# Performance work log

Hardware: AMD Instinct MI355X
Metric: run time of the kernel (lower is better)

## Reference

```python
import jax, jax.numpy as jnp
import numpy as np

EPS = 1e-5  # torch InstanceNorm2d default eps


def conv1x1(x, w, b):
    # x: [B,C,H,W], w: [O,C], b: [O]
    return jnp.einsum('bchw,oc->bohw', x, w) + b[None, :, None, None]


def conv3x3(x, w, b):
    y = jax.lax.conv_general_dilated(x, w, (1, 1), 'SAME',
                                     dimension_numbers=('NCHW', 'OIHW', 'NCHW'))
    return y + b[None, :, None, None]


def inorm(x):
    # InstanceNorm2d, affine=False, biased variance
    m = jnp.mean(x, axis=(2, 3), keepdims=True)
    v = jnp.var(x, axis=(2, 3), keepdims=True)
    return (x - m) * jax.lax.rsqrt(v + EPS)


def self_attn(x, wq, bq, wk, bk, wv, bv, gamma):
    B, C, H, W = x.shape
    N = H * W
    q = conv1x1(x, wq, bq).reshape(B, -1, N)   # [B,C/8,N]
    k = conv1x1(x, wk, bk).reshape(B, -1, N)   # [B,C/8,N]
    A = jax.nn.softmax(jnp.einsum('bdn,bdm->bnm', q, k), axis=-1)  # [B,N,N]
    v = conv1x1(x, wv, bv).reshape(B, C, N)    # [B,C,N]
    out = jnp.einsum('bcm,bnm->bcn', v, A).reshape(B, C, H, W)
    return gamma * out + x


def setup_inputs() -> dict:
    key = jax.random.key(0)
    B, C, H, W = 2, 256, 64, 64
    C8 = C // 8
    ks = iter(jax.random.split(key, 40))

    def n(shape, scale=0.05):
        return jax.random.normal(next(ks), shape, dtype=jnp.float32) * scale

    inp = {
        'x': jax.random.normal(next(ks), (B, C, H, W), dtype=jnp.float32),
        'y': jax.random.normal(next(ks), (B, C, H, W), dtype=jnp.float32),
    }
    for p in ('sa1', 'sa2', 'top'):
        inp[p + '_wq'] = n((C8, C)); inp[p + '_bq'] = n((C8,))
        inp[p + '_wk'] = n((C8, C)); inp[p + '_bk'] = n((C8,))
        inp[p + '_wv'] = n((C, C));  inp[p + '_bv'] = n((C,))
        inp[p + '_gamma'] = n((1,), 0.1)
    inp['conv1_w'] = n((C, C, 3, 3)); inp['conv1_b'] = n((C,))
    inp['conv2_w'] = n((C, C, 3, 3)); inp['conv2_b'] = n((C,))
    return inp


def reference(x, y,
              sa1_wq, sa1_bq, sa1_wk, sa1_bk, sa1_wv, sa1_bv, sa1_gamma,
              sa2_wq, sa2_bq, sa2_wk, sa2_bk, sa2_wv, sa2_bv, sa2_gamma,
              top_wq, top_bq, top_wk, top_bk, top_wv, top_bv, top_gamma,
              conv1_w, conv1_b, conv2_w, conv2_b):
    out_1 = inorm(self_attn(x, sa1_wq, sa1_bq, sa1_wk, sa1_bk, sa1_wv, sa1_bv, sa1_gamma))
    out_2 = inorm(out_1 + conv3x3(out_1, conv1_w, conv1_b))
    out_3 = inorm(self_attn(y, sa2_wq, sa2_bq, sa2_wk, sa2_bk, sa2_wv, sa2_bv, sa2_gamma))

    B, C, H, W = out_2.shape
    N = H * W
    q = conv1x1(out_2, top_wq, top_bq).reshape(B, -1, N)
    k = conv1x1(out_2, top_wk, top_bk).reshape(B, -1, N)
    A = jax.nn.softmax(jnp.einsum('bdn,bdm->bnm', q, k), axis=-1)
    v = conv1x1(out_3, top_wv, top_bv).reshape(B, C, N)
    out = jnp.einsum('bcm,bnm->bcn', v, A).reshape(B, C, H, W)
    out = top_gamma * out + y
    out = inorm(out)
    out = inorm(out + out_3)
    out_4 = conv3x3(out, conv2_w, conv2_b)
    out = inorm(out + out_4)
    return out
```

## Files before the change

### kernel.cpp

```cpp
#include <hip/hip_runtime.h>
#include <hip/hip_bf16.h>

typedef __hip_bfloat16 bf16;
typedef __attribute__((ext_vector_type(8))) short s8v;
typedef __attribute__((ext_vector_type(4))) short s4v;
typedef __attribute__((ext_vector_type(4))) float f4v;

#define NPIX 4096
#define CDIM 256
#define MN_ELEMS (1 << 20)
#define QKVSTR (320L * NPIX)
#define QKTSTR (64L * NPIX)
#define CNL ((long)CDIM * NPIX)

#if __has_builtin(__builtin_amdgcn_exp2f)
#define EXP2F(x) __builtin_amdgcn_exp2f(x)
#else
#define EXP2F(x) exp2f(x)
#endif

typedef __attribute__((address_space(1))) const unsigned int g_u32;
typedef __attribute__((address_space(3))) unsigned int l_u32;
__device__ __forceinline__ void glds16(const void* g, void* l) {
  __builtin_amdgcn_global_load_lds((g_u32*)g, (l_u32*)l, 16, 0, 0);
}

__device__ inline s8v ld8(const bf16* p) { return *(const s8v*)p; }
__device__ inline s8v ld8(const float* p) {
  float4 f0 = *(const float4*)p;
  float4 f1 = *(const float4*)(p + 4);
  s8v r; bf16* e = (bf16*)&r;
  e[0] = __float2bfloat16(f0.x); e[1] = __float2bfloat16(f0.y);
  e[2] = __float2bfloat16(f0.z); e[3] = __float2bfloat16(f0.w);
  e[4] = __float2bfloat16(f1.x); e[5] = __float2bfloat16(f1.y);
  e[6] = __float2bfloat16(f1.z); e[7] = __float2bfloat16(f1.w);
  return r;
}

template<int CB>
__global__ __launch_bounds__(512) void fattn_k(
    const bf16* __restrict__ qkt, const bf16* __restrict__ Vg,
    bf16* __restrict__ out)
{
  constexpr int SC = CB / 64;
  __shared__ bf16 k_s[2][128 * 32];
  __shared__ bf16 v_s[4 * CB * 32];
  __shared__ bf16 p_s[4 * 64 * 32];
  __shared__ float sums[4 * 64];

  const int tid = threadIdx.x;
  const int z = blockIdx.z;
  const int w = tid >> 6, lane = tid & 63;
  const int l15 = lane & 15, oct = lane >> 4;
  const int wr2 = w >> 2, wc2 = w & 3;
  const int pc = w >> 1, pn = w & 1;
  const int n0 = blockIdx.x * 64, c0 = blockIdx.y * CB;
  const bf16* qk = qkt + (long)z * QKTSTR;
  const bf16* Vz = Vg + (long)z * QKVSTR;

  const int t2 = tid >> 2;
  const int kq3 = ((tid & 3) ^ ((t2 >> 1) & 3)) * 8;
  const int vrow = t2 & (CB - 1);
  const int vq3 = ((tid & 3) ^ ((vrow >> 1) & 3)) * 8;

  auto stageK = [&](int m, int buf) {
    glds16(qk + (long)(m + t2) * 64 + 32 + kq3, &k_s[buf][tid * 8]);
  };
  auto stageV = [&](int m) {
    #pragma unroll
    for (int it = 0; it < CB / 32; ++it) {
      const int flat = it * 4096 + tid * 8;
      const int g = flat / (CB * 32);
      glds16(Vz + (long)(c0 + vrow) * 4096 + m + g * 32 + vq3, v_s + flat);
    }
  };

  if (tid < 256)
    glds16(qk + (long)(n0 + t2) * 64 + kq3, p_s + tid * 8);
  stageK(0, 0);
  stageV(0);
  __syncthreads();

  s8v qf[2];
  #pragma unroll
  for (int st = 0; st < 2; ++st) {
    const int row = wr2 * 32 + st * 16 + l15;
    int byte = row * 64 + oct * 16;
    byte ^= ((row >> 1) & 3) << 4;
    qf[st] = *(const s8v*)((const char*)p_s + byte);
  }
  __syncthreads();

  f4v acc[SC][2];
  #pragma unroll
  for (int i = 0; i < SC; ++i)
    #pragma unroll
    for (int j = 0; j < 2; ++j) acc[i][j] = (f4v){0.f, 0.f, 0.f, 0.f};
  float rs[2] = {0.f, 0.f};

  for (int i = 0; i < 32; ++i) {
    const int cur = i & 1;
    if (i < 31) stageK((i + 1) * 128, cur ^ 1);

    s8v kf[2];
    #pragma unroll
    for (int nt = 0; nt < 2; ++nt) {
      const int row = wc2 * 32 + nt * 16 + l15;
      int byte = row * 64 + oct * 16;
      byte ^= ((row >> 1) & 3) << 4;
      kf[nt] = *(const s8v*)((const char*)&k_s[cur][0] + byte);
    }
    #pragma unroll
    for (int st = 0; st < 2; ++st) {
      const int n = wr2 * 32 + st * 16 + l15;
      const int sw = ((n >> 1) & 3) << 4;
      f4v sa[2];
      __builtin_amdgcn_s_setprio(1);
      #pragma unroll
      for (int nt = 0; nt < 2; ++nt) {
        f4v zz = (f4v){0.f, 0.f, 0.f, 0.f};
        sa[nt] = __builtin_amdgcn_mfma_f32_16x16x32_bf16(kf[nt], qf[st], zz, 0, 0, 0);
      }
      __builtin_amdgcn_s_setprio(0);
      #pragma unroll
      for (int nt = 0; nt < 2; ++nt) {
        int byte = wc2 * 4096 + n * 64 + nt * 32 + oct * 8;
        byte ^= sw;
        s4v pk; bf16* pe = (bf16*)&pk;
        float rsum = 0.f;
        #pragma unroll
        for (int r = 0; r < 4; ++r) {
          float e = EXP2F(sa[nt][r]);
          rsum += e;
          pe[r] = __float2bfloat16(e);
        }
        rs[st] += rsum;
        *(s4v*)((char*)p_s + byte) = pk;
      }
    }
    if (i < 31) asm volatile("s_waitcnt vmcnt(1) lgkmcnt(0)" ::: "memory");
    else        asm volatile("s_waitcnt vmcnt(0) lgkmcnt(0)" ::: "memory");
    __builtin_amdgcn_sched_barrier(0);
    __builtin_amdgcn_s_barrier();

    #pragma unroll
    for (int kk = 0; kk < 4; ++kk) {
      s8v vf[SC], pf[2];
      #pragma unroll
      for (int st = 0; st < SC; ++st) {
        const int row = pc * (CB / 4) + st * 16 + l15;
        int byte = kk * (CB * 64) + row * 64 + oct * 16;
        byte ^= ((row >> 1) & 3) << 4;
        vf[st] = *(const s8v*)((const char*)v_s + byte);
      }
      #pragma unroll
      for (int nt = 0; nt < 2; ++nt) {
        const int n = pn * 32 + nt * 16 + l15;
        int byte = kk * 4096 + n * 64 + oct * 16;
        byte ^= ((n >> 1) & 3) << 4;
        pf[nt] = *(const s8v*)((const char*)p_s + byte);
      }
      __builtin_amdgcn_s_setprio(1);
      #pragma unroll
      for (int st = 0; st < SC; ++st)
        #pragma unroll
        for (int nt = 0; nt < 2; ++nt)
          acc[st][nt] = __builtin_amdgcn_mfma_f32_16x16x32_bf16(vf[st], pf[nt], acc[st][nt], 0, 0, 0);
      __builtin_amdgcn_s_setprio(0);
    }
    asm volatile("s_waitcnt vmcnt(0)" ::: "memory");
    __builtin_amdgcn_sched_barrier(0);
    __builtin_amdgcn_s_barrier();

    if (i < 31) stageV((i + 1) * 128);
  }

  #pragma unroll
  for (int st = 0; st < 2; ++st) {
    rs[st] += __shfl_xor(rs[st], 16);
    rs[st] += __shfl_xor(rs[st], 32);
  }
  if (lane < 16) {
    #pragma unroll
    for (int st = 0; st < 2; ++st)
      sums[wc2 * 64 + wr2 * 32 + st * 16 + l15] = rs[st];
  }
  __syncthreads();

  float rinv[2];
  #pragma unroll
  for (int nt = 0; nt < 2; ++nt) {
    const int n = pn * 32 + nt * 16 + l15;
    rinv[nt] = 1.f / (sums[n] + sums[64 + n] + sums[128 + n] + sums[192 + n]);
  }
  bf16* op = out + (long)z * CNL;
  #pragma unroll
  for (int st = 0; st < SC; ++st) {
    const int gc = c0 + pc * (CB / 4) + st * 16 + oct * 4;
    #pragma unroll
    for (int nt = 0; nt < 2; ++nt) {
      const int gn = n0 + pn * 32 + nt * 16 + l15;
      #pragma unroll
      for (int r = 0; r < 4; ++r)
        op[(long)(gc + r) * NPIX + gn] = __float2bfloat16(acc[st][nt][r] * rinv[nt]);
    }
  }
}

__global__ __launch_bounds__(512) void conv_k(
    const bf16* __restrict__ x, const bf16* __restrict__ wcvt,
    const float* __restrict__ bias, bf16* __restrict__ out)
{
  __shared__ bf16 lds[3 * 66 * 66];
  const int tid = threadIdx.x;
  const int h = blockIdx.x;
  const int o0 = blockIdx.y * 128;
  x   += (long)blockIdx.z * CDIM * NPIX;
  out += (long)blockIdx.z * CDIM * NPIX;

  const int w = tid >> 6, lane = tid & 63;
  const int l15 = lane & 15, oct = lane >> 4;

  if (tid < 192) {
    int row = tid >> 6, c = tid & 63;
    lds[(row * 66 + 0) * 66 + c] = __float2bfloat16(0.f);
    lds[(row * 66 + 65) * 66 + c] = __float2bfloat16(0.f);
  }

  f4v acc[4];
  #pragma unroll
  for (int nf = 0; nf < 4; ++nf) acc[nf] = (f4v){0.f, 0.f, 0.f, 0.f};

  const int w2 = tid & 31, chi = tid >> 5;
  const long arow = (long)(o0 + w * 16 + l15) * 2304;

  for (int cg = 0; cg < 4; ++cg) {
    __syncthreads();
    #pragma unroll
    for (int it = 0; it < 12; ++it) {
      int row = it >> 2, cgi = it & 3;
      int c = cgi * 16 + chi;
      int hh = h + row - 1;
      unsigned int pix = 0;
      if ((unsigned)hh < 64u)
        pix = *(const unsigned int*)(x + (long)(cg * 64 + c) * 4096 + hh * 64 + w2 * 2);
      const bf16* pp = (const bf16*)&pix;
      lds[(row * 66 + (w2 * 2 + 1)) * 66 + c] = pp[0];
      lds[(row * 66 + (w2 * 2 + 2)) * 66 + c] = pp[1];
    }
    __syncthreads();

    #pragma unroll
    for (int j = 0; j < 9; ++j) {
      const int dy = j / 3, dx = j % 3;
      #pragma unroll
      for (int kc = 0; kc < 2; ++kc) {
        s8v af = *(const s8v*)(wcvt + arow + j * 256 + cg * 64 + kc * 32 + oct * 8);
        s8v bfv[4];
        #pragma unroll
        for (int nf = 0; nf < 4; ++nf)
          bfv[nf] = *(const s8v*)&lds[(dy * 66 + (nf * 16 + l15 + dx)) * 66 + kc * 32 + oct * 8];
        #pragma unroll
        for (int nf = 0; nf < 4; ++nf)
          acc[nf] = __builtin_amdgcn_mfma_f32_16x16x32_bf16(af, bfv[nf], acc[nf], 0, 0, 0);
      }
    }
  }

  #pragma unroll
  for (int nf = 0; nf < 4; ++nf) {
    const int gn = h * 64 + nf * 16 + l15;
    const int go = o0 + w * 16 + oct * 4;
    #pragma unroll
    for (int r = 0; r < 4; ++r)
      out[(long)(go + r) * NPIX + gn] = __float2bfloat16(acc[nf][r] + bias[go + r]);
  }
}

template<int QKT, typename TBe>
__global__ __launch_bounds__(256) void proj_k(
    const float* __restrict__ A, const float* __restrict__ A2,
    const TBe* __restrict__ B1, const TBe* __restrict__ B2,
    const float* __restrict__ bias, const float* __restrict__ bias2,
    bf16* __restrict__ Cm, bf16* __restrict__ qkt,
    int M, int N, int K, long bbat, long cbat, int nchunk)
{
  __shared__ bf16 a_s[64][40];
  __shared__ bf16 b_s[64][40];
  const int tid = threadIdx.x;
  const int z = blockIdx.z, stage = z >> 1, bat = z & 1;
  const float* Au = stage ? A2 : A;
  const float* biasu = stage ? bias2 : bias;
  const TBe* Bm = (stage ? B2 : B1) + bat * bbat;
  Cm += z * cbat;
  if (QKT) qkt += z * QKTSTR;
  const int m0 = blockIdx.y * 64, n0 = blockIdx.x * 64;
  const int w = tid >> 6, lane = tid & 63;
  const int l15 = lane & 15, oct = lane >> 4;

  f4v acc[4];
  #pragma unroll
  for (int i = 0; i < 4; ++i) acc[i] = (f4v){0.f, 0.f, 0.f, 0.f};

  const int a_i0 = tid >> 2, a_i1 = (tid & 3) * 8;
  const int b_i0 = tid >> 3, b_i1 = (tid & 7) * 8;

  s8v pa, pb;
  auto ldA = [&](int kc, s8v& d) {
    if (m0 + a_i0 < M) d = ld8(Au + (long)(m0 + a_i0) * K + kc * 32 + a_i1);
    else d = (s8v){0,0,0,0,0,0,0,0};
  };
  auto ldB = [&](int kc, s8v& d) {
    d = ld8(Bm + (long)(kc * 32 + b_i0) * N + n0 + b_i1);
  };

  ldA(0, pa); ldB(0, pb);
  for (int kc = 0; kc < nchunk; ++kc) {
    *(s8v*)&a_s[a_i0][a_i1] = pa;
    {
      const bf16* e = (const bf16*)&pb;
      #pragma unroll
      for (int j = 0; j < 8; ++j) b_s[b_i1 + j][b_i0] = e[j];
    }
    __syncthreads();
    if (kc + 1 < nchunk) { ldA(kc + 1, pa); ldB(kc + 1, pb); }
    s8v af = *(const s8v*)&a_s[w * 16 + l15][oct * 8];
    #pragma unroll
    for (int nt = 0; nt < 4; ++nt) {
      s8v bfr = *(const s8v*)&b_s[nt * 16 + l15][oct * 8];
      acc[nt] = __builtin_amdgcn_mfma_f32_16x16x32_bf16(af, bfr, acc[nt], 0, 0, 0);
    }
    __syncthreads();
  }
  const int gm_base = m0 + w * 16 + oct * 4;
  #pragma unroll
  for (int nt = 0; nt < 4; ++nt) {
    const int gn = n0 + nt * 16 + l15;
    #pragma unroll
    for (int r = 0; r < 4; ++r) {
      int gm = gm_base + r;
      if (gm < M) {
        float vv = acc[nt][r] + biasu[gm];
        if (QKT && gm < 64) {
          float vv2 = (gm < 32) ? vv * 1.44269504f : vv;
          qkt[(long)gn * 64 + gm] = __float2bfloat16(vv2);
        } else {
          Cm[(long)gm * N + gn] = __float2bfloat16(vv);
        }
      }
    }
  }
}

__global__ __launch_bounds__(256) void projc_k(
    const float* __restrict__ wqk, const float* __restrict__ bqk,
    const bf16* __restrict__ u2,
    const float* __restrict__ wv, const float* __restrict__ bvv,
    const bf16* __restrict__ u3,
    bf16* __restrict__ qkv, bf16* __restrict__ qkt)
{
  __shared__ bf16 a_s[64][40];
  __shared__ bf16 b_s[64][40];
  const int tid = threadIdx.x;
  const int bat = blockIdx.z;
  const int qkmode = (blockIdx.y == 0);
  const float* Au    = qkmode ? wqk : wv;
  const float* biasu = qkmode ? bqk : bvv;
  const bf16* Bm     = (qkmode ? u2 : u3) + (long)bat * CNL;
  const int M  = qkmode ? 64 : 256;
  const int m0 = qkmode ? 0 : (blockIdx.y - 1) * 64;
  const int n0 = blockIdx.x * 64;
  const int w = tid >> 6, lane = tid & 63;
  const int l15 = lane & 15, oct = lane >> 4;

  f4v acc[4];
  #pragma unroll
  for (int i = 0; i < 4; ++i) acc[i] = (f4v){0.f, 0.f, 0.f, 0.f};

  const int a_i0 = tid >> 2, a_i1 = (tid & 3) * 8;
  const int b_i0 = tid >> 3, b_i1 = (tid & 7) * 8;

  s8v pa, pb;
  auto ldA = [&](int kc, s8v& d) {
    if (m0 + a_i0 < M) d = ld8(Au + (long)(m0 + a_i0) * 256 + kc * 32 + a_i1);
    else d = (s8v){0,0,0,0,0,0,0,0};
  };
  auto ldB = [&](int kc, s8v& d) {
    d = ld8(Bm + (long)(kc * 32 + b_i0) * NPIX + n0 + b_i1);
  };

  ldA(0, pa); ldB(0, pb);
  for (int kc = 0; kc < 8; ++kc) {
    *(s8v*)&a_s[a_i0][a_i1] = pa;
    {
      const bf16* e = (const bf16*)&pb;
      #pragma unroll
      for (int j = 0; j < 8; ++j) b_s[b_i1 + j][b_i0] = e[j];
    }
    __syncthreads();
    if (kc + 1 < 8) { ldA(kc + 1, pa); ldB(kc + 1, pb); }
    s8v af = *(const s8v*)&a_s[w * 16 + l15][oct * 8];
    #pragma unroll
    for (int nt = 0; nt < 4; ++nt) {
      s8v bfr = *(const s8v*)&b_s[nt * 16 + l15][oct * 8];
      acc[nt] = __builtin_amdgcn_mfma_f32_16x16x32_bf16(af, bfr, acc[nt], 0, 0, 0);
    }
    __syncthreads();
  }
  const int gm_base = m0 + w * 16 + oct * 4;
  #pragma unroll
  for (int nt = 0; nt < 4; ++nt) {
    const int gn = n0 + nt * 16 + l15;
    #pragma unroll
    for (int r = 0; r < 4; ++r) {
      int gm = gm_base + r;
      if (gm < M) {
        float vv = acc[nt][r] + biasu[gm];
        if (qkmode) {
          float vv2 = (gm < 32) ? vv * 1.44269504f : vv;
          qkt[(long)bat * QKTSTR + (long)gn * 64 + gm] = __float2bfloat16(vv2);
        } else {
          qkv[64 * NPIX + (long)bat * QKVSTR + (long)gm * NPIX + gn] = __float2bfloat16(vv);
        }
      }
    }
  }
}

__global__ __launch_bounds__(256) void prep_k(
    const float* __restrict__ cw1, const float* __restrict__ cw2,
    bf16* __restrict__ o1, bf16* __restrict__ o2,
    const float* __restrict__ q1, const float* __restrict__ qb1,
    const float* __restrict__ k1, const float* __restrict__ kb1,
    const float* __restrict__ v1, const float* __restrict__ vb1,
    float* __restrict__ wcat1, float* __restrict__ bcat1,
    const float* __restrict__ q2, const float* __restrict__ qb2,
    const float* __restrict__ k2, const float* __restrict__ kb2,
    const float* __restrict__ v2, const float* __restrict__ vb2,
    float* __restrict__ wcat2, float* __restrict__ bcat2,
    const float* __restrict__ qq, const float* __restrict__ qqb,
    const float* __restrict__ kk, const float* __restrict__ kkb,
    float* __restrict__ wqk, float* __restrict__ bqk)
{
  long idx = (long)blockIdx.x * 256 + threadIdx.x;
  if (idx < 1179648) {
    const float* in = (idx < 589824) ? cw1 : cw2;
    bf16* out = (idx < 589824) ? o1 : o2;
    long i = (idx < 589824) ? idx : idx - 589824;
    int o = (int)(i / 2304), r = (int)(i % 2304);
    int j = r >> 8, c = r & 255;
    out[i] = __float2bfloat16(in[(o * 256 + c) * 9 + j]);
    return;
  }
  idx -= 1179648;
  const float *wq, *bq, *wk, *bk, *wv, *bv;
  float *wcat, *bcat; int M;
  if (idx < 82240) {
    wq = q1; bq = qb1; wk = k1; bk = kb1; wv = v1; bv = vb1;
    wcat = wcat1; bcat = bcat1; M = 320;
  } else if (idx < 164480) {
    idx -= 82240;
    wq = q2; bq = qb2; wk = k2; bk = kb2; wv = v2; bv = vb2;
    wcat = wcat2; bcat = bcat2; M = 320;
  } else if (idx < 180928) {
    idx -= 164480;
    wq = qq; bq = qqb; wk = kk; bk = kkb; wv = nullptr; bv = nullptr;
    wcat = wqk; bcat = bqk; M = 64;
  } else return;
  int total = M << 8;
  if (idx < total) {
    int r = (int)(idx >> 8), c = (int)(idx & 255);
    float v;
    if (r < 32) v = wq[r * 256 + c];
    else if (r < 64) v = wk[(r - 32) * 256 + c];
    else v = wv[(r - 64) * 256 + c];
    wcat[idx] = v;
  } else if (idx < total + M) {
    int r = (int)(idx - total);
    bcat[r] = (r < 32) ? bq[r] : (r < 64) ? bk[r - 32] : bv[r - 64];
  }
}

__device__ inline void ld16(const bf16* p, float* v) {
  s8v r0 = *(const s8v*)p, r1 = *(const s8v*)(p + 8);
  const bf16* e0 = (const bf16*)&r0; const bf16* e1 = (const bf16*)&r1;
  #pragma unroll
  for (int j = 0; j < 8; ++j) { v[j] = __bfloat162float(e0[j]); v[8 + j] = __bfloat162float(e1[j]); }
}
__device__ inline void ld16(const float* p, float* v) {
  #pragma unroll
  for (int q = 0; q < 4; ++q) {
    float4 f = *(const float4*)(p + q * 4);
    v[q * 4 + 0] = f.x; v[q * 4 + 1] = f.y; v[q * 4 + 2] = f.z; v[q * 4 + 3] = f.w;
  }
}
__device__ inline void st16(bf16* p, const float* v) {
  s8v o0, o1v; bf16* f0 = (bf16*)&o0; bf16* f1 = (bf16*)&o1v;
  #pragma unroll
  for (int j = 0; j < 8; ++j) { f0[j] = __float2bfloat16(v[j]); f1[j] = __float2bfloat16(v[8 + j]); }
  *(s8v*)p = o0; *(s8v*)(p + 8) = o1v;
}
__device__ inline void st16(float* p, const float* v) {
  #pragma unroll
  for (int q = 0; q < 4; ++q) {
    float4 f; f.x = v[q * 4 + 0]; f.y = v[q * 4 + 1]; f.z = v[q * 4 + 2]; f.w = v[q * 4 + 3];
    *(float4*)(p + q * 4) = f;
  }
}

template<typename TAe, typename TBe, typename TOe, int G>
__global__ __launch_bounds__(256) void inorm_k(
    const TAe* __restrict__ a, const TBe* __restrict__ b,
    const float* __restrict__ g, TOe* __restrict__ out)
{
  __shared__ float red[8];
  const int tid = threadIdx.x;
  const long base = (long)blockIdx.x * NPIX + tid * 16;
  float gv = G ? *g : 1.f;
  float va[16], vbv[16], v[16];
  ld16(a + base, va);
  ld16(b + base, vbv);
  #pragma unroll
  for (int j = 0; j < 16; ++j) v[j] = gv * va[j] + vbv[j];
  float sum = 0.f, sq = 0.f;
  #pragma unroll
  for (int j = 0; j < 16; ++j) { sum += v[j]; sq += v[j] * v[j]; }
  #pragma unroll
  for (int s = 32; s; s >>= 1) { sum += __shfl_xor(sum, s); sq += __shfl_xor(sq, s); }
  if ((tid & 63) == 0) { red[tid >> 6] = sum; red[4 + (tid >> 6)] = sq; }
  __syncthreads();
  sum = red[0] + red[1] + red[2] + red[3];
  sq  = red[4] + red[5] + red[6] + red[7];
  float mean = sum * (1.f / NPIX);
  float var  = fmaxf(sq * (1.f / NPIX) - mean * mean, 0.f);
  float rstd = rsqrtf(var + 1e-5f);
  float o[16];
  #pragma unroll
  for (int j = 0; j < 16; ++j) o[j] = (v[j] - mean) * rstd;
  st16(out + base, o);
}

__global__ __launch_bounds__(256) void inorm2_k(
    const bf16* __restrict__ a0, const float* __restrict__ b0,
    const float* __restrict__ g0, bf16* __restrict__ o0,
    const bf16* __restrict__ a1, const float* __restrict__ b1,
    const float* __restrict__ g1, bf16* __restrict__ o1)
{
  __shared__ float red[8];
  const int tid = threadIdx.x;
  const int sel = blockIdx.x >> 9;
  const int row = blockIdx.x & 511;
  const bf16* a = sel ? a1 : a0;
  const float* b = sel ? b1 : b0;
  const float* g = sel ? g1 : g0;
  bf16* out = sel ? o1 : o0;
  const long base = (long)row * NPIX + tid * 16;
  float gv = *g;
  float va[16], vbv[16], v[16];
  ld16(a + base, va);
  ld16(b + base, vbv);
  #pragma unroll
  for (int j = 0; j < 16; ++j) v[j] = gv * va[j] + vbv[j];
  float sum = 0.f, sq = 0.f;
  #pragma unroll
  for (int j = 0; j < 16; ++j) { sum += v[j]; sq += v[j] * v[j]; }
  #pragma unroll
  for (int s = 32; s; s >>= 1) { sum += __shfl_xor(sum, s); sq += __shfl_xor(sq, s); }
  if ((tid & 63) == 0) { red[tid >> 6] = sum; red[4 + (tid >> 6)] = sq; }
  __syncthreads();
  sum = red[0] + red[1] + red[2] + red[3];
  sq  = red[4] + red[5] + red[6] + red[7];
  float mean = sum * (1.f / NPIX);
  float var  = fmaxf(sq * (1.f / NPIX) - mean * mean, 0.f);
  float rstd = rsqrtf(var + 1e-5f);
  float o[16];
  #pragma unroll
  for (int j = 0; j < 16; ++j) o[j] = (v[j] - mean) * rstd;
  st16(out + base, o);
}

static const long CN = CNL;

static void attn_core(int nb, bf16* qkv, bf16* qkt, bf16* t0, hipStream_t stream)
{
  if (nb == 4)
    fattn_k<128><<<dim3(64, 2, 4), dim3(512), 0, stream>>>(qkt, qkv + 64 * NPIX, t0);
  else
    fattn_k<64><<<dim3(64, 4, 2), dim3(512), 0, stream>>>(qkt, qkv + 64 * NPIX, t0);
}

static void run_conv(const bf16* src, const bf16* wcvt, const float* cb,
                     bf16* dst, hipStream_t stream)
{
  conv_k<<<dim3(64, 2, 2), dim3(512), 0, stream>>>(src, wcvt, cb, dst);
}

extern "C" void kernel_launch(void* const* d_in, const int* in_sizes, int n_in,
                              void* d_out, int out_size, void* d_ws, size_t ws_size,
                              hipStream_t stream)
{
  (void)in_sizes; (void)n_in; (void)out_size; (void)ws_size;
  const float* x = (const float*)d_in[0];
  const float* y = (const float*)d_in[1];
  auto W = [&](int i) { return (const float*)d_in[i]; };

  char* wp = (char*)d_ws;
  auto take = [&](size_t nbytes) { char* p = wp; wp += (nbytes + 255) & ~(size_t)255; return p; };
  bf16*  qkv   = (bf16*)take((size_t)4 * QKVSTR * 2);
  bf16*  qkt   = (bf16*)take((size_t)4 * QKTSTR * 2);
  bf16*  t0    = (bf16*)take((size_t)4 * CN * 2);
  bf16*  u1    = (bf16*)take(2 * CN * 2);
  bf16*  u2    = (bf16*)take(2 * CN * 2);
  bf16*  u3    = (bf16*)take(2 * CN * 2);
  bf16*  u4    = (bf16*)take(2 * CN * 2);
  bf16*  wcvt1 = (bf16*)take((size_t)589824 * 2);
  bf16*  wcvt2 = (bf16*)take((size_t)589824 * 2);
  float* wcat1 = (float*)take((size_t)81920 * 4);
  float* bcat1 = (float*)take(320 * 4);
  float* wcat2 = (float*)take((size_t)81920 * 4);
  float* bcat2 = (float*)take(320 * 4);
  float* wqk   = (float*)take((size_t)16384 * 4);
  float* bqk   = (float*)take(64 * 4);
  bf16*  cvout = qkv;

  dim3 TB(256);

  prep_k<<<dim3(5315), TB, 0, stream>>>(
      W(23), W(25), wcvt1, wcvt2,
      W(2), W(3), W(4), W(5), W(6), W(7), wcat1, bcat1,
      W(9), W(10), W(11), W(12), W(13), W(14), wcat2, bcat2,
      W(16), W(17), W(18), W(19), wqk, bqk);

  proj_k<1,float><<<dim3(64,5,4), TB, 0, stream>>>(
      wcat1, wcat2, x, y, bcat1, bcat2, qkv, qkt, 320, NPIX, 256, CN, QKVSTR, 8);
  attn_core(4, qkv, qkt, t0, stream);

  inorm2_k<<<dim3(1024), TB, 0, stream>>>(t0, x, W(8), u1,
                                          t0 + 2 * CN, y, W(15), u3);

  run_conv(u1, wcvt1, W(24), cvout, stream);
  inorm_k<bf16,bf16,bf16,0><<<dim3(512), TB, 0, stream>>>(u1, cvout, nullptr, u2);

  projc_k<<<dim3(64, 5, 2), TB, 0, stream>>>(
      wqk, bqk, u2, W(20), W(21), u3, qkv, qkt);
  attn_core(2, qkv, qkt, t0, stream);
  inorm_k<bf16,float,bf16,1><<<dim3(512), TB, 0, stream>>>(t0, y, W(22), u1);
  inorm_k<bf16,bf16,bf16,0><<<dim3(512), TB, 0, stream>>>(u1, u3, nullptr, u4);
  run_conv(u4, wcvt2, W(26), cvout, stream);
  inorm_k<bf16,bf16,float,0><<<dim3(512), TB, 0, stream>>>(u4, cvout, nullptr, (float*)d_out);
}
```

Before: 337.7 us.

## Double-buffer conv LDS staging, swizzle projection B tile, fuse paired inorms

The 3x3 conv kernel now uses two LDS buffers, so the next channel group is staged while MFMAs run on the current one, with one barrier per group. The transposed B-tile writes in both projection kernels use an XOR byte swizzle to reduce LDS bank conflicts. The two back-to-back instance norms after the top attention are fused into one kernel, which removes an intermediate bf16 round trip and a launch. Double buffering doubles the conv kernel's LDS use (about 52 KB per block), which may lower occupancy.

```diff
diff --git a/kernel.cpp b/kernel.cpp
--- a/kernel.cpp
+++ b/kernel.cpp
@@ -211,7 +211,7 @@
     const bf16* __restrict__ x, const bf16* __restrict__ wcvt,
     const float* __restrict__ bias, bf16* __restrict__ out)
 {
-  __shared__ bf16 lds[3 * 66 * 66];
+  __shared__ bf16 lds[2][3 * 66 * 66];
   const int tid = threadIdx.x;
   const int h = blockIdx.x;
   const int o0 = blockIdx.y * 128;
@@ -220,22 +220,18 @@
 
   const int w = tid >> 6, lane = tid & 63;
   const int l15 = lane & 15, oct = lane >> 4;
+  const int w2 = tid & 31, chi = tid >> 5;
 
   if (tid < 192) {
     int row = tid >> 6, c = tid & 63;
-    lds[(row * 66 + 0) * 66 + c] = __float2bfloat16(0.f);
-    lds[(row * 66 + 65) * 66 + c] = __float2bfloat16(0.f);
-  }
-
-  f4v acc[4];
-  #pragma unroll
-  for (int nf = 0; nf < 4; ++nf) acc[nf] = (f4v){0.f, 0.f, 0.f, 0.f};
-
-  const int w2 = tid & 31, chi = tid >> 5;
-  const long arow = (long)(o0 + w * 16 + l15) * 2304;
-
-  for (int cg = 0; cg < 4; ++cg) {
-    __syncthreads();
+    #pragma unroll
+    for (int b = 0; b < 2; ++b) {
+      lds[b][(row * 66 + 0) * 66 + c] = __float2bfloat16(0.f);
+      lds[b][(row * 66 + 65) * 66 + c] = __float2bfloat16(0.f);
+    }
+  }
+
+  auto stage = [&](int cg, bf16* dst) {
     #pragma unroll
     for (int it = 0; it < 12; ++it) {
       int row = it >> 2, cgi = it & 3;
@@ -245,11 +241,24 @@
       if ((unsigned)hh < 64u)
         pix = *(const unsigned int*)(x + (long)(cg * 64 + c) * 4096 + hh * 64 + w2 * 2);
       const bf16* pp = (const bf16*)&pix;
-      lds[(row * 66 + (w2 * 2 + 1)) * 66 + c] = pp[0];
-      lds[(row * 66 + (w2 * 2 + 2)) * 66 + c] = pp[1];
-    }
-    __syncthreads();
-
+      dst[(row * 66 + (w2 * 2 + 1)) * 66 + c] = pp[0];
+      dst[(row * 66 + (w2 * 2 + 2)) * 66 + c] = pp[1];
+    }
+  };
+
+  f4v acc[4];
+  #pragma unroll
+  for (int nf = 0; nf < 4; ++nf) acc[nf] = (f4v){0.f, 0.f, 0.f, 0.f};
+
+  const long arow = (long)(o0 + w * 16 + l15) * 2304;
+
+  stage(0, &lds[0][0]);
+  __syncthreads();
+
+  #pragma unroll
+  for (int cg = 0; cg < 4; ++cg) {
+    if (cg < 3) stage(cg + 1, &lds[(cg + 1) & 1][0]);
+    const bf16* cl = &lds[cg & 1][0];
     #pragma unroll
     for (int j = 0; j < 9; ++j) {
       const int dy = j / 3, dx = j % 3;
@@ -259,12 +268,13 @@
         s8v bfv[4];
         #pragma unroll
         for (int nf = 0; nf < 4; ++nf)
-          bfv[nf] = *(const s8v*)&lds[(dy * 66 + (nf * 16 + l15 + dx)) * 66 + kc * 32 + oct * 8];
+          bfv[nf] = *(const s8v*)&cl[(dy * 66 + (nf * 16 + l15 + dx)) * 66 + kc * 32 + oct * 8];
         #pragma unroll
         for (int nf = 0; nf < 4; ++nf)
           acc[nf] = __builtin_amdgcn_mfma_f32_16x16x32_bf16(af, bfv[nf], acc[nf], 0, 0, 0);
       }
     }
+    __syncthreads();
   }
 
   #pragma unroll
@@ -275,6 +285,10 @@
     for (int r = 0; r < 4; ++r)
       out[(long)(go + r) * NPIX + gn] = __float2bfloat16(acc[nf][r] + bias[go + r]);
   }
+}
+
+__device__ __forceinline__ int bswz(int row, int byteInRow) {
+  return row * 80 + (byteInRow ^ (((row >> 3) & 3) << 4));
 }
 
 template<int QKT, typename TBe>
@@ -320,14 +334,15 @@
     {
       const bf16* e = (const bf16*)&pb;
       #pragma unroll
-      for (int j = 0; j < 8; ++j) b_s[b_i1 + j][b_i0] = e[j];
+      for (int j = 0; j < 8; ++j)
+        *(bf16*)((char*)b_s + bswz(b_i1 + j, 2 * b_i0)) = e[j];
     }
     __syncthreads();
     if (kc + 1 < nchunk) { ldA(kc + 1, pa); ldB(kc + 1, pb); }
     s8v af = *(const s8v*)&a_s[w * 16 + l15][oct * 8];
     #pragma unroll
     for (int nt = 0; nt < 4; ++nt) {
-      s8v bfr = *(const s8v*)&b_s[nt * 16 + l15][oct * 8];
+      s8v bfr = *(const s8v*)((const char*)b_s + bswz(nt * 16 + l15, oct * 16));
       acc[nt] = __builtin_amdgcn_mfma_f32_16x16x32_bf16(af, bfr, acc[nt], 0, 0, 0);
     }
     __syncthreads();
@@ -395,14 +410,15 @@
     {
       const bf16* e = (const bf16*)&pb;
       #pragma unroll
-      for (int j = 0; j < 8; ++j) b_s[b_i1 + j][b_i0] = e[j];
+      for (int j = 0; j < 8; ++j)
+        *(bf16*)((char*)b_s + bswz(b_i1 + j, 2 * b_i0)) = e[j];
     }
     __syncthreads();
     if (kc + 1 < 8) { ldA(kc + 1, pa); ldB(kc + 1, pb); }
     s8v af = *(const s8v*)&a_s[w * 16 + l15][oct * 8];
     #pragma unroll
     for (int nt = 0; nt < 4; ++nt) {
-      s8v bfr = *(const s8v*)&b_s[nt * 16 + l15][oct * 8];
+      s8v bfr = *(const s8v*)((const char*)b_s + bswz(nt * 16 + l15, oct * 16));
       acc[nt] = __builtin_amdgcn_mfma_f32_16x16x32_bf16(af, bfr, acc[nt], 0, 0, 0);
     }
     __syncthreads();
@@ -579,6 +595,54 @@
   st16(out + base, o);
 }
 
+__global__ __launch_bounds__(256) void inorm_pair_k(
+    const bf16* __restrict__ t0, const float* __restrict__ y,
+    const float* __restrict__ g, const bf16* __restrict__ u3,
+    bf16* __restrict__ u4)
+{
+  __shared__ float red[16];
+  const int tid = threadIdx.x;
+  const long base = (long)blockIdx.x * NPIX + tid * 16;
+  float gv = *g;
+  float va[16], vbv[16], v[16];
+  ld16(t0 + base, va);
+  ld16(y + base, vbv);
+  #pragma unroll
+  for (int j = 0; j < 16; ++j) v[j] = gv * va[j] + vbv[j];
+  float sum = 0.f, sq = 0.f;
+  #pragma unroll
+  for (int j = 0; j < 16; ++j) { sum += v[j]; sq += v[j] * v[j]; }
+  #pragma unroll
+  for (int s = 32; s; s >>= 1) { sum += __shfl_xor(sum, s); sq += __shfl_xor(sq, s); }
+  if ((tid & 63) == 0) { red[tid >> 6] = sum; red[4 + (tid >> 6)] = sq; }
+  __syncthreads();
+  sum = red[0] + red[1] + red[2] + red[3];
+  sq  = red[4] + red[5] + red[6] + red[7];
+  float mean = sum * (1.f / NPIX);
+  float var  = fmaxf(sq * (1.f / NPIX) - mean * mean, 0.f);
+  float rstd = rsqrtf(var + 1e-5f);
+  float vu[16];
+  ld16(u3 + base, vu);
+  #pragma unroll
+  for (int j = 0; j < 16; ++j) v[j] = (v[j] - mean) * rstd + vu[j];
+  sum = 0.f; sq = 0.f;
+  #pragma unroll
+  for (int j = 0; j < 16; ++j) { sum += v[j]; sq += v[j] * v[j]; }
+  #pragma unroll
+  for (int s = 32; s; s >>= 1) { sum += __shfl_xor(sum, s); sq += __shfl_xor(sq, s); }
+  if ((tid & 63) == 0) { red[8 + (tid >> 6)] = sum; red[12 + (tid >> 6)] = sq; }
+  __syncthreads();
+  sum = red[8] + red[9] + red[10] + red[11];
+  sq  = red[12] + red[13] + red[14] + red[15];
+  mean = sum * (1.f / NPIX);
+  var  = fmaxf(sq * (1.f / NPIX) - mean * mean, 0.f);
+  rstd = rsqrtf(var + 1e-5f);
+  float o[16];
+  #pragma unroll
+  for (int j = 0; j < 16; ++j) o[j] = (v[j] - mean) * rstd;
+  st16(u4 + base, o);
+}
+
 static const long CN = CNL;
 
 static void attn_core(int nb, bf16* qkv, bf16* qkt, bf16* t0, hipStream_t stream)
@@ -644,8 +708,7 @@
   projc_k<<<dim3(64, 5, 2), TB, 0, stream>>>(
       wqk, bqk, u2, W(20), W(21), u3, qkv, qkt);
   attn_core(2, qkv, qkt, t0, stream);
-  inorm_k<bf16,float,bf16,1><<<dim3(512), TB, 0, stream>>>(t0, y, W(22), u1);
-  inorm_k<bf16,bf16,bf16,0><<<dim3(512), TB, 0, stream>>>(u1, u3, nullptr, u4);
+  inorm_pair_k<<<dim3(512), TB, 0, stream>>>(t0, y, W(22), u3, u4);
   run_conv(u4, wcvt2, W(26), cvout, stream);
   inorm_k<bf16,bf16,float,0><<<dim3(512), TB, 0, stream>>>(u4, cvout, nullptr, (float*)d_out);
 }
```

New measurement: 414.7 us. 22.8% more time.
